# Performance work log

Measured on AMD Instinct MI355X. Metric: run time of the kernel, lower is better.

Reference implementation:

```python
import jax, jax.numpy as jnp
import numpy as np
import math

DIM = 1024
N_HEAD = 16
HEAD_DIM = DIM // N_HEAD  # 64
B, T = 4, 2048


def rotate_half(x):
    # lucidrains-style interleaved rotation: (x1, x2) pairs -> (-x2, x1)
    x = x.reshape(*x.shape[:-1], -1, 2)
    x1, x2 = x[..., 0], x[..., 1]
    return jnp.stack((-x2, x1), axis=-1).reshape(*x.shape[:-2], -1)


def apply_rope(x):
    # x: [b, h, t, d]
    d = x.shape[-1]
    t = x.shape[-2]
    inv_freq = 1.0 / (10000.0 ** (jnp.arange(0, d, 2, dtype=jnp.float32) / d))  # [d/2]
    angles = jnp.arange(t, dtype=jnp.float32)[:, None] * inv_freq[None, :]      # [t, d/2]
    angles = jnp.repeat(angles, 2, axis=-1)                                     # [t, d] interleaved
    cos, sin = jnp.cos(angles), jnp.sin(angles)
    return x * cos + rotate_half(x) * sin


def setup_inputs() -> dict:
    key = jax.random.key(0)
    kx, kw1, kb1, kw2, kb2 = jax.random.split(key, 5)
    x = jax.random.normal(kx, (B, T, DIM), dtype=jnp.float32)
    mask = jnp.tril(jnp.ones((T, T), dtype=jnp.int32))  # causal
    s = 0.02
    qkv_w = jax.random.normal(kw1, (DIM, 3 * DIM), dtype=jnp.float32) * s
    qkv_b = jax.random.normal(kb1, (3 * DIM,), dtype=jnp.float32) * s
    out_w = jax.random.normal(kw2, (DIM, DIM), dtype=jnp.float32) * s
    out_b = jax.random.normal(kb2, (DIM,), dtype=jnp.float32) * s
    return {"x": x, "mask": mask, "qkv_w": qkv_w, "qkv_b": qkv_b,
            "out_w": out_w, "out_b": out_b}


def reference(x, mask, qkv_w, qkv_b, out_w, out_b):
    b, t, _ = x.shape
    qkv = x @ qkv_w + qkv_b                       # [b, t, 3*dim]
    q, k, v = jnp.split(qkv, 3, axis=-1)
    def to_heads(z):
        return z.reshape(b, t, N_HEAD, HEAD_DIM).transpose(0, 2, 1, 3)  # [b,h,t,d]
    q, k, v = to_heads(q), to_heads(k), to_heads(v)
    q = apply_rope(q)
    k = apply_rope(k)
    scores = jnp.einsum('bhqd,bhkd->bhqk', q, k) / math.sqrt(HEAD_DIM)
    scores = jnp.where(mask[None, None, :, :] == 0, -jnp.inf, scores)
    attn = jax.nn.softmax(scores, axis=-1)        # dropout = identity (eval)
    out = jnp.einsum('bhqk,bhkd->bhqd', attn, v)  # [b,h,t,d]
    out = out.transpose(0, 2, 1, 3).reshape(b, t, DIM)
    return out @ out_w + out_b
```

## Files before the change

kernel.cpp:

```cpp
#include <hip/hip_runtime.h>

typedef __bf16 bf16_t;
typedef __bf16 bf16x8 __attribute__((ext_vector_type(8)));
typedef float  f32x4  __attribute__((ext_vector_type(4)));
typedef float  f32x16 __attribute__((ext_vector_type(16)));
typedef unsigned u32x4 __attribute__((ext_vector_type(4)));

#define DIMM  1024
#define NHEAD 16
#define HDIM  64
#define BATCH 4
#define SEQ   2048
#define MROWS (BATCH*SEQ)

#define AQB   128
#define AKV   64
#define NP    (SEQ/AQB)
#define SKS   72
#define LOG2E 1.44269504088896f

__device__ const int d_qb[24] = {15,15,7,14,14,13,13,6,12,12,11,11,5,10,10,9,9,4,8,8,3,2,1,0};
__device__ const int d_hh[24] = { 0, 1,2, 0, 1, 0, 1,2, 0, 1, 0, 1,2, 0, 1,0,1,2,0,1,2,2,2,2};

__device__ __forceinline__ void gload_lds16(const bf16_t* g, bf16_t* l) {
  __builtin_amdgcn_global_load_lds(
      (const __attribute__((address_space(1))) void*)g,
      (__attribute__((address_space(3))) void*)l, 16, 0, 0);
}

__device__ __forceinline__ unsigned short f2bu(float f) {
  bf16_t b = (bf16_t)f;
  return __builtin_bit_cast(unsigned short, b);
}
__device__ __forceinline__ float bu2f(unsigned short u) {
  return __uint_as_float(((unsigned)u) << 16);
}
__device__ __forceinline__ unsigned packbf(float a, float b) {
  return (unsigned)f2bu(a) | ((unsigned)f2bu(b) << 16);
}
__device__ __forceinline__ float fexp2(float x) {
  float r; asm("v_exp_f32 %0, %1" : "=v"(r) : "v"(x)); return r;
}

__global__ void k_convert(const float* __restrict__ in, bf16_t* __restrict__ out, int n4,
                          float* __restrict__ cosT, float* __restrict__ sinT) {
  int i = blockIdx.x * blockDim.x + threadIdx.x;
  if (i < n4) {
    float4 v = reinterpret_cast<const float4*>(in)[i];
    ushort4 o;
    o.x = f2bu(v.x); o.y = f2bu(v.y); o.z = f2bu(v.z); o.w = f2bu(v.w);
    reinterpret_cast<ushort4*>(out)[i] = o;
  } else {
    int id = i - n4;
    if (id < SEQ * 32) {
      int t = id >> 5, j = id & 31;
      double ang = (double)t * pow(10000.0, -(double)j / 32.0);
      cosT[id] = (float)cos(ang);
      sinT[id] = (float)sin(ang);
    }
  }
}

__global__ void k_transpose_convert(const float* __restrict__ in, bf16_t* __restrict__ out,
                                    int R, int C) {
  __shared__ float tile[32][33];
  int cb = blockIdx.x * 32, rb = blockIdx.y * 32;
  int tx = threadIdx.x, ty = threadIdx.y;
  #pragma unroll
  for (int i = 0; i < 4; ++i)
    tile[ty + i*8][tx] = in[(size_t)(rb + ty + i*8) * C + cb + tx];
  __syncthreads();
  #pragma unroll
  for (int i = 0; i < 4; ++i)
    out[(size_t)(cb + ty + i*8) * R + rb + tx] = (bf16_t)tile[tx][ty + i*8];
}

__global__ __launch_bounds__(512, 2) void k_gemm0(
    const bf16_t* __restrict__ A, const bf16_t* __restrict__ BT,
    const float* __restrict__ bias,
    bf16_t* __restrict__ q, bf16_t* __restrict__ k, bf16_t* __restrict__ vt,
    const float* __restrict__ cosT, const float* __restrict__ sinT)
{
  __shared__ bf16_t sA[2][2][128 * 64];
  __shared__ bf16_t sB[2][2][128 * 64];

  const int tid = threadIdx.x;
  const int w = tid >> 6;
  const int lane = tid & 63;
  const int wm = w >> 2, wn = w & 3;
  const int l15 = lane & 15, l4 = lane >> 4;

  int nwg = gridDim.x * gridDim.y;
  int id  = blockIdx.y * gridDim.x + blockIdx.x;
  int cpx = nwg >> 3;
  int sid = (id & 7) * cpx + (id >> 3);
  int bx = sid % gridDim.x, by = sid / gridDim.x;
  const int rowA0 = by * 256, colB0 = bx * 256;

  f32x4 acc[8][4] = {};
  bf16x8 bf_[4];

  auto stage = [&](int tile, int part) {
    if (tile >= 16) return;
    const int kh = part >> 1;
    const bool isB = part & 1;
    const bf16_t* src = isB ? BT : A;
    const int r0 = isB ? colB0 : rowA0;
    bf16_t* dst = (isB ? &sB[0][0][0] : &sA[0][0][0]) + ((tile & 1) * 2 + kh) * (128 * 64);
    #pragma unroll
    for (int call = 0; call < 2; ++call) {
      int n = call * 512 + tid;
      int R = n >> 3, slot = n & 7;
      int sp = slot ^ (R & 7);
      int row = R * 2 + (sp >> 2);
      gload_lds16(src + (size_t)(r0 + row) * 1024 + tile * 64 + kh * 32 + (sp & 3) * 8,
                  dst + n * 8);
    }
  };

  auto rdA = [&](int bc, int kh, int mfa) -> bf16x8 {
    int row = wm * 128 + mfa * 16 + l15;
    int R = row >> 1;
    int slot = (((row & 1) << 2) | l4) ^ (R & 7);
    return *reinterpret_cast<const bf16x8*>(&sA[bc][kh][R * 64 + slot * 8]);
  };
  auto rdB = [&](int bc, int kh, int nf) -> bf16x8 {
    int row = wn * 64 + nf * 16 + l15;
    int R = row >> 1;
    int slot = (((row & 1) << 2) | l4) ^ (R & 7);
    return *reinterpret_cast<const bf16x8*>(&sB[bc][kh][R * 64 + slot * 8]);
  };

  auto phase = [&](int bc, int kh, int mh, int stile, int spart, int wait_n) {
    bf16x8 af[4];
    if (mh == 0) {
      #pragma unroll
      for (int nf = 0; nf < 4; ++nf) bf_[nf] = rdB(bc, kh, nf);
    }
    #pragma unroll
    for (int mf = 0; mf < 4; ++mf) af[mf] = rdA(bc, kh, mh * 4 + mf);
    stage(stile, spart);
    if (wait_n == 4)      asm volatile("s_waitcnt vmcnt(4)" ::: "memory");
    else if (wait_n == 0) asm volatile("s_waitcnt vmcnt(0)" ::: "memory");
    __builtin_amdgcn_s_barrier();
    __builtin_amdgcn_s_setprio(1);
    #pragma unroll
    for (int mf = 0; mf < 4; ++mf)
      #pragma unroll
      for (int nf = 0; nf < 4; ++nf)
        acc[mh * 4 + mf][nf] = __builtin_amdgcn_mfma_f32_16x16x32_bf16(
            af[mf], bf_[nf], acc[mh * 4 + mf][nf], 0, 0, 0);
    __builtin_amdgcn_s_setprio(0);
    __builtin_amdgcn_s_barrier();
  };

  stage(0, 0); stage(0, 1); stage(0, 2); stage(0, 3);
  stage(1, 0); stage(1, 1);
  asm volatile("s_waitcnt vmcnt(4)" ::: "memory");
  __builtin_amdgcn_s_barrier();

  for (int i = 0; i < 8; ++i) {
    const int t0 = 2 * i, t1 = 2 * i + 1;
    phase(0, 0, 0, t1,     2, -1);
    phase(0, 0, 1, t1,     3, -1);
    phase(0, 1, 0, t0 + 2, 0, -1);
    phase(0, 1, 1, t0 + 2, 1, (t0 + 2 < 16) ? 4 : 0);
    phase(1, 0, 0, t0 + 2, 2, -1);
    phase(1, 0, 1, t0 + 2, 3, -1);
    phase(1, 1, 0, t0 + 3, 0, -1);
    phase(1, 1, 1, t0 + 3, 1, (t0 + 3 < 16) ? 4 : 0);
  }

  const bool isV = (bx >= 8);
  const bool isQ = (bx < 4);
  const float qs = 0.125f * LOG2E;
  if (isV) {
    #pragma unroll
    for (int mfa = 0; mfa < 8; ++mfa) {
      #pragma unroll
      for (int nf = 0; nf < 4; ++nf) {
        int n = colB0 + wn * 64 + nf * 16 + l15;
        int h = (n >> 6) & 15, d = n & 63;
        float bs = bias[n];
        int m0 = rowA0 + wm * 128 + mfa * 16 + l4 * 4;
        int b = m0 >> 11, t = m0 & 2047;
        ushort4 pk;
        pk.x = f2bu(acc[mfa][nf][0] + bs);
        pk.y = f2bu(acc[mfa][nf][1] + bs);
        pk.z = f2bu(acc[mfa][nf][2] + bs);
        pk.w = f2bu(acc[mfa][nf][3] + bs);
        *reinterpret_cast<ushort4*>(
            vt + ((size_t)((b * NHEAD + h) * HDIM + d)) * SEQ + t) = pk;
      }
    }
  } else {
    bf16_t* dst = isQ ? q : k;
    #pragma unroll
    for (int mfa = 0; mfa < 8; ++mfa) {
      #pragma unroll
      for (int nf = 0; nf < 4; ++nf) {
        int n = colB0 + wn * 64 + nf * 16 + l15;
        int h = (n >> 6) & 15, d = n & 63;
        int i2 = d >> 1;
        float bs = bias[n];
        #pragma unroll
        for (int r = 0; r < 4; ++r) {
          int m = rowA0 + wm * 128 + mfa * 16 + l4 * 4 + r;
          int b = m >> 11, t = m & 2047;
          float val = acc[mfa][nf][r] + bs;
          float prt = __shfl_xor(val, 1);
          float c = cosT[(t << 5) + i2], s = sinT[(t << 5) + i2];
          float y = (d & 1) ? (val * c + prt * s) : (val * c - prt * s);
          if (isQ) y *= qs;
          dst[((size_t)(b * NHEAD + h) * SEQ + t) * HDIM + d] = (bf16_t)y;
        }
      }
    }
  }
}

__global__ __launch_bounds__(256) void k_gemm1(
    const bf16_t* __restrict__ A, const bf16_t* __restrict__ BT,
    const float* __restrict__ bias, float* __restrict__ outf, int M, int N, int K)
{
  __shared__ bf16_t sA[128 * 32];
  __shared__ bf16_t sB[128 * 32];
  const int tid = threadIdx.x;
  const int w = tid >> 6, lane = tid & 63;
  const int wr = w >> 1, wc = w & 1;
  const int l15 = lane & 15, l4 = lane >> 4;

  int nwg = gridDim.x * gridDim.y;
  int id  = blockIdx.y * gridDim.x + blockIdx.x;
  int cpx = nwg >> 3;
  int sid = (id & 7) * cpx + (id >> 3);
  int bx = sid % gridDim.x, by = sid / gridDim.x;

  const int rowA0 = by * 128;
  const int colB0 = bx * 128;

  f32x4 acc[4][4] = {};

  const int nkt = K >> 5;
  for (int kt = 0; kt < nkt; ++kt) {
    __syncthreads();
    #pragma unroll
    for (int i = 0; i < 2; ++i) {
      int c = i * 256 + w * 64 + lane;
      int row = c >> 2, k8 = (c & 3) * 8;
      gload_lds16(A  + (size_t)(rowA0 + row) * K + kt * 32 + k8, sA + (i * 256 + w * 64) * 8);
      gload_lds16(BT + (size_t)(colB0 + row) * K + kt * 32 + k8, sB + (i * 256 + w * 64) * 8);
    }
    asm volatile("s_waitcnt vmcnt(0)" ::: "memory");
    __syncthreads();
    bf16x8 af[4], bfr[4];
    #pragma unroll
    for (int mi = 0; mi < 4; ++mi)
      af[mi] = *reinterpret_cast<const bf16x8*>(sA + (wr * 64 + mi * 16 + l15) * 32 + l4 * 8);
    #pragma unroll
    for (int ni = 0; ni < 4; ++ni)
      bfr[ni] = *reinterpret_cast<const bf16x8*>(sB + (wc * 64 + ni * 16 + l15) * 32 + l4 * 8);
    #pragma unroll
    for (int mi = 0; mi < 4; ++mi)
      #pragma unroll
      for (int ni = 0; ni < 4; ++ni)
        acc[mi][ni] = __builtin_amdgcn_mfma_f32_16x16x32_bf16(af[mi], bfr[ni], acc[mi][ni], 0, 0, 0);
  }

  #pragma unroll
  for (int mi = 0; mi < 4; ++mi) {
    #pragma unroll
    for (int ni = 0; ni < 4; ++ni) {
      int n = colB0 + wc * 64 + ni * 16 + l15;
      float bs = bias[n];
      #pragma unroll
      for (int r = 0; r < 4; ++r) {
        int m = rowA0 + wr * 64 + mi * 16 + l4 * 4 + r;
        outf[(size_t)m * N + n] = acc[mi][ni][r] + bs;
      }
    }
  }
}

#define ATTN_BODY(CBUF, T)                                                     \
  do {                                                                         \
    const int t_ = (T);                                                        \
    if (t_ + 1 < t1) {                                                         \
      asm volatile("s_waitcnt vmcnt(0)" ::: "memory");                         \
      stage(CBUF ^ 1);                                                         \
      if (t_ + 2 < t1) issue(t_ + 2);                                          \
    }                                                                          \
    const bool masked = (t_ * AKV + AKV - 1 > qbase);                          \
    f32x16 s0 = {}, s1 = {};                                                   \
    __builtin_amdgcn_s_setprio(1);                                             \
    _Pragma("unroll")                                                          \
    for (int kt = 0; kt < 4; ++kt) {                                           \
      bf16x8 kf0 = *reinterpret_cast<const bf16x8*>(                           \
          &sK[CBUF][l31 * SKS + (((2 * kt + hi) ^ (l31 >> 3)) << 3)]);         \
      s0 = __builtin_amdgcn_mfma_f32_32x32x16_bf16(kf0, qf[kt], s0, 0, 0, 0);  \
    }                                                                          \
    _Pragma("unroll")                                                          \
    for (int kt = 0; kt < 4; ++kt) {                                           \
      int kr1 = 32 + l31;                                                      \
      bf16x8 kf1 = *reinterpret_cast<const bf16x8*>(                           \
          &sK[CBUF][kr1 * SKS + (((2 * kt + hi) ^ (kr1 >> 3)) << 3)]);         \
      s1 = __builtin_amdgcn_mfma_f32_32x32x16_bf16(kf1, qf[kt], s1, 0, 0, 0);  \
    }                                                                          \
    __builtin_amdgcn_s_setprio(0);                                             \
    const int qa = qbase + l31;                                                \
    const int kb0 = t_ * AKV + 4 * hi;                                         \
    if (masked) {                                                              \
      _Pragma("unroll")                                                        \
      for (int r = 0; r < 16; ++r) {                                           \
        int kvi = kb0 + (r & 3) + 8 * (r >> 2);                                \
        if (kvi > qa) s0[r] = -1e30f;                                          \
        if (kvi + 32 > qa) s1[r] = -1e30f;                                     \
      }                                                                        \
    }                                                                          \
    float mm[16];                                                              \
    _Pragma("unroll")                                                          \
    for (int r = 0; r < 16; ++r) mm[r] = fmaxf(s0[r], s1[r]);                  \
    float m0_ = fmaxf(fmaxf(mm[0],  mm[1]),  mm[2]);                           \
    float m1_ = fmaxf(fmaxf(mm[3],  mm[4]),  mm[5]);                           \
    float m2_ = fmaxf(fmaxf(mm[6],  mm[7]),  mm[8]);                           \
    float m3_ = fmaxf(fmaxf(mm[9],  mm[10]), mm[11]);                          \
    float m4_ = fmaxf(fmaxf(mm[12], mm[13]), mm[14]);                          \
    float mt = fmaxf(fmaxf(fmaxf(m0_, m1_), fmaxf(m2_, m3_)), fmaxf(m4_, mm[15])); \
    mt = fmaxf(mt, __shfl_xor(mt, 32));                                        \
    if (!__all(mt <= mrun + 11.54f)) {                                         \
      float mnew = fmaxf(mrun, mt);                                            \
      float scl = fexp2(mrun - mnew);                                          \
      mrun = mnew;                                                             \
      lrun *= scl;                                                             \
      _Pragma("unroll")                                                        \
      for (int i = 0; i < 16; ++i) { accO[0][i] *= scl; accO[1][i] *= scl; }   \
    }                                                                          \
    float rs = 0.f;                                                            \
    _Pragma("unroll")                                                          \
    for (int r = 0; r < 16; ++r) { s0[r] = fexp2(s0[r] - mrun); rs += s0[r]; } \
    _Pragma("unroll")                                                          \
    for (int r = 0; r < 16; ++r) { s1[r] = fexp2(s1[r] - mrun); rs += s1[r]; } \
    lrun += rs;            \
    bf16x8 pf[4];                                                              \
    _Pragma("unroll")                                                          \
    for (int ktt = 0; ktt < 4; ++ktt) {                                        \
      const int bb = 8 * (ktt & 1);                                            \
      unsigned P01, P23, P45, P67;                                             \
      if (ktt < 2) {                                                           \
        P01 = packbf(s0[bb+0], s0[bb+1]); P23 = packbf(s0[bb+2], s0[bb+3]);    \
        P45 = packbf(s0[bb+4], s0[bb+5]); P67 = packbf(s0[bb+6], s0[bb+7]);    \
      } else {                                                                 \
        P01 = packbf(s1[bb+0], s1[bb+1]); P23 = packbf(s1[bb+2], s1[bb+3]);    \
        P45 = packbf(s1[bb+4], s1[bb+5]); P67 = packbf(s1[bb+6], s1[bb+7]);    \
      }                                                                        \
      unsigned ra = __shfl_xor(hi == 0 ? P45 : P01, 32);                       \
      unsigned rb = __shfl_xor(hi == 0 ? P67 : P23, 32);                       \
      unsigned dw0 = hi == 0 ? P01 : ra;                                       \
      unsigned dw1 = hi == 0 ? P23 : rb;                                       \
      unsigned dw2 = hi == 0 ? ra : P45;                                       \
      unsigned dw3 = hi == 0 ? rb : P67;                                       \
      pf[ktt] = __builtin_bit_cast(bf16x8, (u32x4){dw0, dw1, dw2, dw3});       \
    }                                                                          \
    __builtin_amdgcn_s_setprio(1);                                             \
    _Pragma("unroll")                                                          \
    for (int dt = 0; dt < 2; ++dt) {                                           \
      _Pragma("unroll")                                                        \
      for (int ktt = 0; ktt < 4; ++ktt) {                                      \
        int vrow = 32 * dt + l31;                                              \
        int slot = (4 * (ktt >> 1) + 2 * (ktt & 1) + hi) ^ (vrow >> 3);        \
        bf16x8 vf = *reinterpret_cast<const bf16x8*>(                          \
            &sV[CBUF][vrow * SKS + (slot << 3)]);                              \
        accO[dt] = __builtin_amdgcn_mfma_f32_32x32x16_bf16(vf, pf[ktt], accO[dt], 0, 0, 0); \
      }                                                                        \
    }                                                                          \
    __builtin_amdgcn_s_setprio(0);                                             \
    asm volatile("s_waitcnt lgkmcnt(0)" ::: "memory");                         \
    __builtin_amdgcn_s_barrier();                                              \
    asm volatile("" ::: "memory");                                             \
  } while (0)

__global__ __launch_bounds__(256, 2) void k_attn(
    const bf16_t* __restrict__ Q, const bf16_t* __restrict__ Kb,
    const bf16_t* __restrict__ Vt, bf16_t* __restrict__ O,
    bf16_t* __restrict__ Opart, float* __restrict__ ml)
{
  __shared__ bf16_t sK[2][64 * SKS];
  __shared__ bf16_t sV[2][64 * SKS];

  const int tid = threadIdx.x;
  const int w = tid >> 6, lane = tid & 63;
  const int l31 = lane & 31, hi = lane >> 5;

  const int id = blockIdx.x;
  const int cls = id >> 6;
  const int bh = id & 63;
  const int qblk = d_qb[cls];
  const int hh = d_hh[cls];
  const int ntf = 2 * qblk + 2;
  const int t0 = (hh == 1) ? (ntf >> 1) : 0;
  const int t1 = (hh == 0) ? (ntf >> 1) : ntf;

  const size_t hbase = (size_t)bh * SEQ * HDIM;
  const int b = bh >> 4, h = bh & 15;
  const int srow = tid >> 3, sslot = tid & 7;

  const int qbase = qblk * AQB + 32 * w;

  bf16x8 qf[4];
  #pragma unroll
  for (int kt = 0; kt < 4; ++kt)
    qf[kt] = *reinterpret_cast<const bf16x8*>(
        Q + hbase + (size_t)(qbase + l31) * HDIM + kt * 16 + hi * 8);
  asm volatile("s_waitcnt vmcnt(0)" ::: "memory");
  asm volatile("" : "+v"(qf[0]), "+v"(qf[1]), "+v"(qf[2]), "+v"(qf[3]));

  u32x4 kr[2], vr[2];
  auto issue = [&](int t) {
    const bf16_t* kp = Kb + hbase + (size_t)(t * AKV + srow) * HDIM + sslot * 8;
    const bf16_t* vp = Vt + hbase + (size_t)srow * SEQ + t * AKV + sslot * 8;
    asm volatile("global_load_dwordx4 %0, %1, off" : "=v"(kr[0]) : "v"(kp));
    asm volatile("global_load_dwordx4 %0, %1, off" : "=v"(kr[1]) : "v"(kp + 32 * HDIM));
    asm volatile("global_load_dwordx4 %0, %1, off" : "=v"(vr[0]) : "v"(vp));
    asm volatile("global_load_dwordx4 %0, %1, off" : "=v"(vr[1]) : "v"(vp + 32 * SEQ));
  };
  auto stage = [&](int nb) {
    #pragma unroll
    for (int cc = 0; cc < 2; ++cc) {
      int row = srow + 32 * cc;
      *reinterpret_cast<u32x4*>(&sK[nb][row * SKS + ((sslot ^ (row >> 3)) << 3)]) = kr[cc];
      *reinterpret_cast<u32x4*>(&sV[nb][row * SKS + ((sslot ^ (row >> 3)) << 3)]) = vr[cc];
    }
  };

  float mrun = -1e30f, lrun = 0.f;
  f32x16 accO[2] = {};

  issue(t0);
  asm volatile("s_waitcnt vmcnt(0)" ::: "memory");
  stage(0);
  if (t0 + 1 < t1) issue(t0 + 1);
  asm volatile("s_waitcnt lgkmcnt(0)" ::: "memory");
  __builtin_amdgcn_s_barrier();
  asm volatile("" ::: "memory");

  int t = t0;
  if ((t1 - t0) & 1) {
    ATTN_BODY(0, t); ++t;
    for (; t < t1; t += 2) { ATTN_BODY(1, t); ATTN_BODY(0, t + 1); }
  } else {
    for (; t < t1; t += 2) { ATTN_BODY(0, t); ATTN_BODY(1, t + 1); }
  }

  lrun += __shfl_xor(lrun, 32);

  bf16_t* sOw = &sK[0][0] + w * (32 * SKS);
  float inv = 1.f / lrun;
  #pragma unroll
  for (int dt = 0; dt < 2; ++dt)
    #pragma unroll
    for (int r = 0; r < 16; ++r) {
      int d = 32 * dt + (r & 3) + 8 * (r >> 2) + 4 * hi;
      sOw[l31 * SKS + (d ^ ((l31 >> 3) << 3))] = (bf16_t)(accO[dt][r] * inv);
    }
  if (hh == 2) {
    #pragma unroll
    for (int i = 0; i < 4; ++i) {
      int qr = 8 * i + (lane >> 3);
      int ch = lane & 7;
      bf16x8 vvv = *reinterpret_cast<const bf16x8*>(
          &sOw[qr * SKS + ((ch ^ (qr >> 3)) << 3)]);
      *reinterpret_cast<bf16x8*>(
          O + ((size_t)(b * SEQ + qbase + qr)) * DIMM + h * HDIM + ch * 8) = vvv;
    }
  } else {
    const int pb = ((qblk - 8) * 2 + hh) * 64 + bh;
    #pragma unroll
    for (int i = 0; i < 4; ++i) {
      int qr = 8 * i + (lane >> 3);
      int ch = lane & 7;
      bf16x8 vvv = *reinterpret_cast<const bf16x8*>(
          &sOw[qr * SKS + ((ch ^ (qr >> 3)) << 3)]);
      *reinterpret_cast<bf16x8*>(
          Opart + ((size_t)pb * 128 + 32 * w + qr) * 64 + ch * 8) = vvv;
    }
    if (hi == 0) {
      size_t mi = ((size_t)pb * 128 + 32 * w + l31) * 2;
      ml[mi] = mrun; ml[mi + 1] = lrun;
    }
  }
}

__global__ __launch_bounds__(256) void k_merge(
    const bf16_t* __restrict__ Opart, const float* __restrict__ ml,
    bf16_t* __restrict__ O)
{
  int blk = blockIdx.x;
  int qi = blk >> 6;
  int bh = blk & 63;
  int b = bh >> 4, h = bh & 15;
  int qblk = qi + 8;
  int base0 = (qi * 2 + 0) * 64 + bh;
  int base1 = (qi * 2 + 1) * 64 + bh;
  int q = threadIdx.x >> 1;
  int d0 = (threadIdx.x & 1) * 32;

  float m0 = ml[((size_t)base0 * 128 + q) * 2], l0 = ml[((size_t)base0 * 128 + q) * 2 + 1];
  float m1 = ml[((size_t)base1 * 128 + q) * 2], l1 = ml[((size_t)base1 * 128 + q) * 2 + 1];
  float m = fmaxf(m0, m1);
  float w0 = fexp2(m0 - m) * l0;
  float w1 = fexp2(m1 - m) * l1;
  float inv = 1.f / (w0 + w1);
  w0 *= inv; w1 *= inv;

  const bf16_t* p0 = Opart + ((size_t)base0 * 128 + q) * 64 + d0;
  const bf16_t* p1 = Opart + ((size_t)base1 * 128 + q) * 64 + d0;
  bf16_t* po = O + ((size_t)(b * SEQ + qblk * 128 + q)) * DIMM + h * HDIM + d0;
  #pragma unroll
  for (int i = 0; i < 4; ++i) {
    bf16x8 a = *reinterpret_cast<const bf16x8*>(p0 + i * 8);
    bf16x8 c = *reinterpret_cast<const bf16x8*>(p1 + i * 8);
    bf16x8 o;
    #pragma unroll
    for (int j = 0; j < 8; ++j)
      o[j] = (bf16_t)(w0 * (float)a[j] + w1 * (float)c[j]);
    *reinterpret_cast<bf16x8*>(po + i * 8) = o;
  }
}

extern "C" void kernel_launch(void* const* d_in, const int* in_sizes, int n_in,
                              void* d_out, int out_size, void* d_ws, size_t ws_size,
                              hipStream_t stream) {
  const float* x     = (const float*)d_in[0];
  const float* qkv_w = (const float*)d_in[2];
  const float* qkv_b = (const float*)d_in[3];
  const float* out_w = (const float*)d_in[4];
  const float* out_b = (const float*)d_in[5];
  float* out = (float*)d_out;

  char* ws = (char*)d_ws;
  size_t off = 0;
  auto alloc = [&](size_t bytes) {
    char* p = ws + off;
    off += (bytes + 255) & ~(size_t)255;
    return (void*)p;
  };
  bf16_t* Xb    = (bf16_t*)alloc((size_t)MROWS * DIMM * 2);
  bf16_t* WqkvT = (bf16_t*)alloc((size_t)3 * DIMM * DIMM * 2);
  bf16_t* WoutT = (bf16_t*)alloc((size_t)DIMM * DIMM * 2);
  bf16_t* Qh    = (bf16_t*)alloc((size_t)64 * SEQ * HDIM * 2);
  bf16_t* Kh    = (bf16_t*)alloc((size_t)64 * SEQ * HDIM * 2);
  bf16_t* Vth   = (bf16_t*)alloc((size_t)64 * HDIM * SEQ * 2);
  bf16_t* AO    = (bf16_t*)alloc((size_t)MROWS * DIMM * 2);
  float*  cosT  = (float*)alloc((size_t)SEQ * 32 * 4);
  float*  sinT  = (float*)alloc((size_t)SEQ * 32 * 4);
  float*  mlbuf = (float*)alloc((size_t)16 * 64 * 128 * 2 * 4);
  bf16_t* Opart = Xb;

  const int n4 = MROWS * DIMM / 4;
  k_convert<<<(n4 + SEQ * 32 + 255) / 256, 256, 0, stream>>>(x, Xb, n4, cosT, sinT);
  k_transpose_convert<<<dim3(3 * DIMM / 32, DIMM / 32), dim3(32, 8), 0, stream>>>(qkv_w, WqkvT, DIMM, 3 * DIMM);
  k_transpose_convert<<<dim3(DIMM / 32, DIMM / 32), dim3(32, 8), 0, stream>>>(out_w, WoutT, DIMM, DIMM);

  k_gemm0<<<dim3(3 * DIMM / 256, MROWS / 256), 512, 0, stream>>>(
      Xb, WqkvT, qkv_b, Qh, Kh, Vth, cosT, sinT);

  k_attn<<<dim3(24 * 64), 256, 0, stream>>>(Qh, Kh, Vth, AO, Opart, mlbuf);

  k_merge<<<dim3(512), 256, 0, stream>>>(Opart, mlbuf, AO);

  k_gemm1<<<dim3(DIMM / 128, MROWS / 128), 256, 0, stream>>>(
      AO, WoutT, out_b, out, MROWS, DIMM, DIMM);
}
```

Measured before the change: 193.4 us.

## Interleave two paired attention work items per block to overlap softmax and MFMA

Each attention block now processes two complementary (q-block, split) work classes at once, chosen from a pairing table so the two items' combined KV tile counts are roughly balanced. Each item gets its own double-buffered K/V LDS tiles, Q fragments, running max/sum and accumulators. Per iteration the QK MFMAs of both streams are issued before their softmax and PV phases, so one stream's exp/max work can overlap the other's matrix ops. The grid is halved, and one barrier is shared per iteration. In exchange, LDS use per block doubles and register pressure rises sharply under launch_bounds(256,2), which risks spills or lower occupancy.

```diff
diff --git a/kernel.cpp b/kernel.cpp
--- a/kernel.cpp
+++ b/kernel.cpp
@@ -21,6 +21,7 @@
 
 __device__ const int d_qb[24] = {15,15,7,14,14,13,13,6,12,12,11,11,5,10,10,9,9,4,8,8,3,2,1,0};
 __device__ const int d_hh[24] = { 0, 1,2, 0, 1, 0, 1,2, 0, 1, 0, 1,2, 0, 1,0,1,2,0,1,2,2,2,2};
+__device__ const int d_pa[12] = {4,6,7,9,11,3,5,8,10,2,1,0};
 
 __device__ __forceinline__ void gload_lds16(const bf16_t* g, bf16_t* l) {
   __builtin_amdgcn_global_load_lds(
@@ -282,101 +283,155 @@
   }
 }
 
-#define ATTN_BODY(CBUF, T)                                                     \
+#define ISSUE_J(krj, vrj, tj)                                                  \
   do {                                                                         \
-    const int t_ = (T);                                                        \
-    if (t_ + 1 < t1) {                                                         \
-      asm volatile("s_waitcnt vmcnt(0)" ::: "memory");                         \
-      stage(CBUF ^ 1);                                                         \
-      if (t_ + 2 < t1) issue(t_ + 2);                                          \
-    }                                                                          \
-    const bool masked = (t_ * AKV + AKV - 1 > qbase);                          \
-    f32x16 s0 = {}, s1 = {};                                                   \
+    const bf16_t* kp_ = Kb + hbase + (size_t)((tj) * AKV + srow) * HDIM + sslot * 8; \
+    const bf16_t* vp_ = Vt + hbase + (size_t)srow * SEQ + (tj) * AKV + sslot * 8; \
+    asm volatile("global_load_dwordx4 %0, %1, off" : "=v"(krj[0]) : "v"(kp_)); \
+    asm volatile("global_load_dwordx4 %0, %1, off" : "=v"(krj[1]) : "v"(kp_ + 32 * HDIM)); \
+    asm volatile("global_load_dwordx4 %0, %1, off" : "=v"(vrj[0]) : "v"(vp_)); \
+    asm volatile("global_load_dwordx4 %0, %1, off" : "=v"(vrj[1]) : "v"(vp_ + 32 * SEQ)); \
+  } while (0)
+
+#define STAGE_J(sKj, sVj, nb, krj, vrj)                                        \
+  do {                                                                         \
+    _Pragma("unroll")                                                          \
+    for (int cc_ = 0; cc_ < 2; ++cc_) {                                        \
+      int row_ = srow + 32 * cc_;                                              \
+      *reinterpret_cast<u32x4*>(&sKj[nb][row_ * SKS + ((sslot ^ (row_ >> 3)) << 3)]) = krj[cc_]; \
+      *reinterpret_cast<u32x4*>(&sVj[nb][row_ * SKS + ((sslot ^ (row_ >> 3)) << 3)]) = vrj[cc_]; \
+    }                                                                          \
+  } while (0)
+
+#define QK_J(sKj, cb, qfj, s0j, s1j)                                           \
+  do {                                                                         \
     __builtin_amdgcn_s_setprio(1);                                             \
     _Pragma("unroll")                                                          \
-    for (int kt = 0; kt < 4; ++kt) {                                           \
-      bf16x8 kf0 = *reinterpret_cast<const bf16x8*>(                           \
-          &sK[CBUF][l31 * SKS + (((2 * kt + hi) ^ (l31 >> 3)) << 3)]);         \
-      s0 = __builtin_amdgcn_mfma_f32_32x32x16_bf16(kf0, qf[kt], s0, 0, 0, 0);  \
-    }                                                                          \
-    _Pragma("unroll")                                                          \
-    for (int kt = 0; kt < 4; ++kt) {                                           \
-      int kr1 = 32 + l31;                                                      \
-      bf16x8 kf1 = *reinterpret_cast<const bf16x8*>(                           \
-          &sK[CBUF][kr1 * SKS + (((2 * kt + hi) ^ (kr1 >> 3)) << 3)]);         \
-      s1 = __builtin_amdgcn_mfma_f32_32x32x16_bf16(kf1, qf[kt], s1, 0, 0, 0);  \
+    for (int kt_ = 0; kt_ < 4; ++kt_) {                                        \
+      bf16x8 kf_ = *reinterpret_cast<const bf16x8*>(                           \
+          &sKj[cb][l31 * SKS + (((2 * kt_ + hi) ^ (l31 >> 3)) << 3)]);         \
+      s0j = __builtin_amdgcn_mfma_f32_32x32x16_bf16(kf_, qfj[kt_], s0j, 0, 0, 0); \
+    }                                                                          \
+    _Pragma("unroll")                                                          \
+    for (int kt_ = 0; kt_ < 4; ++kt_) {                                        \
+      int kr_ = 32 + l31;                                                      \
+      bf16x8 kf_ = *reinterpret_cast<const bf16x8*>(                           \
+          &sKj[cb][kr_ * SKS + (((2 * kt_ + hi) ^ (kr_ >> 3)) << 3)]);         \
+      s1j = __builtin_amdgcn_mfma_f32_32x32x16_bf16(kf_, qfj[kt_], s1j, 0, 0, 0); \
     }                                                                          \
     __builtin_amdgcn_s_setprio(0);                                             \
-    const int qa = qbase + l31;                                                \
-    const int kb0 = t_ * AKV + 4 * hi;                                         \
-    if (masked) {                                                              \
+  } while (0)
+
+#define SMPV_J(sVj, cb, tj, qbasej, s0j, s1j, mrunj, lrunj, accj)              \
+  do {                                                                         \
+    const bool masked_ = ((tj) * AKV + AKV - 1 > (qbasej));                    \
+    const int qa_ = (qbasej) + l31;                                            \
+    const int kb0_ = (tj) * AKV + 4 * hi;                                      \
+    if (masked_) {                                                             \
       _Pragma("unroll")                                                        \
-      for (int r = 0; r < 16; ++r) {                                           \
-        int kvi = kb0 + (r & 3) + 8 * (r >> 2);                                \
-        if (kvi > qa) s0[r] = -1e30f;                                          \
-        if (kvi + 32 > qa) s1[r] = -1e30f;                                     \
-      }                                                                        \
-    }                                                                          \
-    float mm[16];                                                              \
-    _Pragma("unroll")                                                          \
-    for (int r = 0; r < 16; ++r) mm[r] = fmaxf(s0[r], s1[r]);                  \
-    float m0_ = fmaxf(fmaxf(mm[0],  mm[1]),  mm[2]);                           \
-    float m1_ = fmaxf(fmaxf(mm[3],  mm[4]),  mm[5]);                           \
-    float m2_ = fmaxf(fmaxf(mm[6],  mm[7]),  mm[8]);                           \
-    float m3_ = fmaxf(fmaxf(mm[9],  mm[10]), mm[11]);                          \
-    float m4_ = fmaxf(fmaxf(mm[12], mm[13]), mm[14]);                          \
-    float mt = fmaxf(fmaxf(fmaxf(m0_, m1_), fmaxf(m2_, m3_)), fmaxf(m4_, mm[15])); \
-    mt = fmaxf(mt, __shfl_xor(mt, 32));                                        \
-    if (!__all(mt <= mrun + 11.54f)) {                                         \
-      float mnew = fmaxf(mrun, mt);                                            \
-      float scl = fexp2(mrun - mnew);                                          \
-      mrun = mnew;                                                             \
-      lrun *= scl;                                                             \
+      for (int r_ = 0; r_ < 16; ++r_) {                                        \
+        int kvi_ = kb0_ + (r_ & 3) + 8 * (r_ >> 2);                            \
+        if (kvi_ > qa_) s0j[r_] = -1e30f;                                      \
+        if (kvi_ + 32 > qa_) s1j[r_] = -1e30f;                                 \
+      }                                                                        \
+    }                                                                          \
+    float mm_[16];                                                             \
+    _Pragma("unroll")                                                          \
+    for (int r_ = 0; r_ < 16; ++r_) mm_[r_] = fmaxf(s0j[r_], s1j[r_]);         \
+    float a0_ = fmaxf(fmaxf(mm_[0],  mm_[1]),  mm_[2]);                        \
+    float a1_ = fmaxf(fmaxf(mm_[3],  mm_[4]),  mm_[5]);                        \
+    float a2_ = fmaxf(fmaxf(mm_[6],  mm_[7]),  mm_[8]);                        \
+    float a3_ = fmaxf(fmaxf(mm_[9],  mm_[10]), mm_[11]);                       \
+    float a4_ = fmaxf(fmaxf(mm_[12], mm_[13]), mm_[14]);                       \
+    float mt_ = fmaxf(fmaxf(fmaxf(a0_, a1_), fmaxf(a2_, a3_)), fmaxf(a4_, mm_[15])); \
+    mt_ = fmaxf(mt_, __shfl_xor(mt_, 32));                                     \
+    if (!__all(mt_ <= mrunj + 11.54f)) {                                       \
+      float mn_ = fmaxf(mrunj, mt_);                                           \
+      float sc_ = fexp2(mrunj - mn_);                                          \
+      mrunj = mn_;                                                             \
+      lrunj *= sc_;                                                            \
       _Pragma("unroll")                                                        \
-      for (int i = 0; i < 16; ++i) { accO[0][i] *= scl; accO[1][i] *= scl; }   \
-    }                                                                          \
-    float rs = 0.f;                                                            \
-    _Pragma("unroll")                                                          \
-    for (int r = 0; r < 16; ++r) { s0[r] = fexp2(s0[r] - mrun); rs += s0[r]; } \
-    _Pragma("unroll")                                                          \
-    for (int r = 0; r < 16; ++r) { s1[r] = fexp2(s1[r] - mrun); rs += s1[r]; } \
-    lrun += rs;            \
-    bf16x8 pf[4];                                                              \
-    _Pragma("unroll")                                                          \
-    for (int ktt = 0; ktt < 4; ++ktt) {                                        \
-      const int bb = 8 * (ktt & 1);                                            \
-      unsigned P01, P23, P45, P67;                                             \
-      if (ktt < 2) {                                                           \
-        P01 = packbf(s0[bb+0], s0[bb+1]); P23 = packbf(s0[bb+2], s0[bb+3]);    \
-        P45 = packbf(s0[bb+4], s0[bb+5]); P67 = packbf(s0[bb+6], s0[bb+7]);    \
+      for (int i_ = 0; i_ < 16; ++i_) { accj[0][i_] *= sc_; accj[1][i_] *= sc_; } \
+    }                                                                          \
+    float rs_ = 0.f;                                                           \
+    _Pragma("unroll")                                                          \
+    for (int r_ = 0; r_ < 16; ++r_) { s0j[r_] = fexp2(s0j[r_] - mrunj); rs_ += s0j[r_]; } \
+    _Pragma("unroll")                                                          \
+    for (int r_ = 0; r_ < 16; ++r_) { s1j[r_] = fexp2(s1j[r_] - mrunj); rs_ += s1j[r_]; } \
+    lrunj += rs_;                                                              \
+    bf16x8 pf_[4];                                                             \
+    _Pragma("unroll")                                                          \
+    for (int kt_ = 0; kt_ < 4; ++kt_) {                                        \
+      const int bb_ = 8 * (kt_ & 1);                                           \
+      unsigned P01_, P23_, P45_, P67_;                                         \
+      if (kt_ < 2) {                                                           \
+        P01_ = packbf(s0j[bb_+0], s0j[bb_+1]); P23_ = packbf(s0j[bb_+2], s0j[bb_+3]); \
+        P45_ = packbf(s0j[bb_+4], s0j[bb_+5]); P67_ = packbf(s0j[bb_+6], s0j[bb_+7]); \
       } else {                                                                 \
-        P01 = packbf(s1[bb+0], s1[bb+1]); P23 = packbf(s1[bb+2], s1[bb+3]);    \
-        P45 = packbf(s1[bb+4], s1[bb+5]); P67 = packbf(s1[bb+6], s1[bb+7]);    \
-      }                                                                        \
-      unsigned ra = __shfl_xor(hi == 0 ? P45 : P01, 32);                       \
-      unsigned rb = __shfl_xor(hi == 0 ? P67 : P23, 32);                       \
-      unsigned dw0 = hi == 0 ? P01 : ra;                                       \
-      unsigned dw1 = hi == 0 ? P23 : rb;                                       \
-      unsigned dw2 = hi == 0 ? ra : P45;                                       \
-      unsigned dw3 = hi == 0 ? rb : P67;                                       \
-      pf[ktt] = __builtin_bit_cast(bf16x8, (u32x4){dw0, dw1, dw2, dw3});       \
+        P01_ = packbf(s1j[bb_+0], s1j[bb_+1]); P23_ = packbf(s1j[bb_+2], s1j[bb_+3]); \
+        P45_ = packbf(s1j[bb_+4], s1j[bb_+5]); P67_ = packbf(s1j[bb_+6], s1j[bb_+7]); \
+      }                                                                        \
+      unsigned ra_ = __shfl_xor(hi == 0 ? P45_ : P01_, 32);                    \
+      unsigned rb_ = __shfl_xor(hi == 0 ? P67_ : P23_, 32);                    \
+      unsigned d0_ = hi == 0 ? P01_ : ra_;                                     \
+      unsigned d1_ = hi == 0 ? P23_ : rb_;                                     \
+      unsigned d2_ = hi == 0 ? ra_ : P45_;                                     \
+      unsigned d3_ = hi == 0 ? rb_ : P67_;                                     \
+      pf_[kt_] = __builtin_bit_cast(bf16x8, (u32x4){d0_, d1_, d2_, d3_});      \
     }                                                                          \
     __builtin_amdgcn_s_setprio(1);                                             \
     _Pragma("unroll")                                                          \
-    for (int dt = 0; dt < 2; ++dt) {                                           \
+    for (int dt_ = 0; dt_ < 2; ++dt_) {                                        \
       _Pragma("unroll")                                                        \
-      for (int ktt = 0; ktt < 4; ++ktt) {                                      \
-        int vrow = 32 * dt + l31;                                              \
-        int slot = (4 * (ktt >> 1) + 2 * (ktt & 1) + hi) ^ (vrow >> 3);        \
-        bf16x8 vf = *reinterpret_cast<const bf16x8*>(                          \
-            &sV[CBUF][vrow * SKS + (slot << 3)]);                              \
-        accO[dt] = __builtin_amdgcn_mfma_f32_32x32x16_bf16(vf, pf[ktt], accO[dt], 0, 0, 0); \
+      for (int kt_ = 0; kt_ < 4; ++kt_) {                                      \
+        int vr_ = 32 * dt_ + l31;                                              \
+        int sl_ = (4 * (kt_ >> 1) + 2 * (kt_ & 1) + hi) ^ (vr_ >> 3);          \
+        bf16x8 vf_ = *reinterpret_cast<const bf16x8*>(                         \
+            &sVj[cb][vr_ * SKS + (sl_ << 3)]);                                 \
+        accj[dt_] = __builtin_amdgcn_mfma_f32_32x32x16_bf16(vf_, pf_[kt_], accj[dt_], 0, 0, 0); \
       }                                                                        \
     }                                                                          \
     __builtin_amdgcn_s_setprio(0);                                             \
+  } while (0)
+
+#define EPI_J(hhj, qbj, qbasej, mrunj, lrunj, accj)                            \
+  do {                                                                         \
+    lrunj += __shfl_xor(lrunj, 32);                                            \
+    float inv_ = 1.f / lrunj;                                                  \
+    _Pragma("unroll")                                                          \
+    for (int dt_ = 0; dt_ < 2; ++dt_)                                          \
+      _Pragma("unroll")                                                        \
+      for (int r_ = 0; r_ < 16; ++r_) {                                        \
+        int d_ = 32 * dt_ + (r_ & 3) + 8 * (r_ >> 2) + 4 * hi;                 \
+        sOw[l31 * SKS + (d_ ^ ((l31 >> 3) << 3))] = (bf16_t)(accj[dt_][r_] * inv_); \
+      }                                                                        \
+    if ((hhj) == 2) {                                                          \
+      _Pragma("unroll")                                                        \
+      for (int i_ = 0; i_ < 4; ++i_) {                                         \
+        int qr_ = 8 * i_ + (lane >> 3);                                        \
+        int ch_ = lane & 7;                                                    \
+        bf16x8 vv_ = *reinterpret_cast<const bf16x8*>(                         \
+            &sOw[qr_ * SKS + ((ch_ ^ (qr_ >> 3)) << 3)]);                      \
+        *reinterpret_cast<bf16x8*>(                                            \
+            O + ((size_t)(b * SEQ + (qbasej) + qr_)) * DIMM + h * HDIM + ch_ * 8) = vv_; \
+      }                                                                        \
+    } else {                                                                   \
+      const int pb_ = (((qbj) - 8) * 2 + (hhj)) * 64 + bh;                     \
+      _Pragma("unroll")                                                        \
+      for (int i_ = 0; i_ < 4; ++i_) {                                         \
+        int qr_ = 8 * i_ + (lane >> 3);                                        \
+        int ch_ = lane & 7;                                                    \
+        bf16x8 vv_ = *reinterpret_cast<const bf16x8*>(                         \
+            &sOw[qr_ * SKS + ((ch_ ^ (qr_ >> 3)) << 3)]);                      \
+        *reinterpret_cast<bf16x8*>(                                            \
+            Opart + ((size_t)pb_ * 128 + 32 * w + qr_) * 64 + ch_ * 8) = vv_;  \
+      }                                                                        \
+      if (hi == 0) {                                                           \
+        size_t mi_ = ((size_t)pb_ * 128 + 32 * w + l31) * 2;                   \
+        ml[mi_] = mrunj; ml[mi_ + 1] = lrunj;                                  \
+      }                                                                        \
+    }                                                                          \
     asm volatile("s_waitcnt lgkmcnt(0)" ::: "memory");                         \
-    __builtin_amdgcn_s_barrier();                                              \
-    asm volatile("" ::: "memory");                                             \
   } while (0)
 
 __global__ __launch_bounds__(256, 2) void k_attn(
@@ -384,110 +439,79 @@
     const bf16_t* __restrict__ Vt, bf16_t* __restrict__ O,
     bf16_t* __restrict__ Opart, float* __restrict__ ml)
 {
-  __shared__ bf16_t sK[2][64 * SKS];
-  __shared__ bf16_t sV[2][64 * SKS];
+  __shared__ bf16_t sKA[2][64 * SKS], sVA[2][64 * SKS];
+  __shared__ bf16_t sKB[2][64 * SKS], sVB[2][64 * SKS];
 
   const int tid = threadIdx.x;
   const int w = tid >> 6, lane = tid & 63;
   const int l31 = lane & 31, hi = lane >> 5;
-
-  const int id = blockIdx.x;
-  const int cls = id >> 6;
-  const int bh = id & 63;
-  const int qblk = d_qb[cls];
-  const int hh = d_hh[cls];
-  const int ntf = 2 * qblk + 2;
-  const int t0 = (hh == 1) ? (ntf >> 1) : 0;
-  const int t1 = (hh == 0) ? (ntf >> 1) : ntf;
+  const int srow = tid >> 3, sslot = tid & 7;
+
+  const int pr = blockIdx.x >> 6, bh = blockIdx.x & 63;
+  const int clsA = d_pa[pr], clsB = 23 - clsA;
+  const int qbA = d_qb[clsA], hhA = d_hh[clsA];
+  const int qbB = d_qb[clsB], hhB = d_hh[clsB];
+  const int ntA = 2 * qbA + 2, ntB = 2 * qbB + 2;
+  const int t0A = (hhA == 1) ? (ntA >> 1) : 0;
+  const int t1A = (hhA == 0) ? (ntA >> 1) : ntA;
+  const int t0B = (hhB == 1) ? (ntB >> 1) : 0;
+  const int t1B = (hhB == 0) ? (ntB >> 1) : ntB;
+  const int nA = t1A - t0A, nB = t1B - t0B;
+  const int nmax = nA > nB ? nA : nB;
 
   const size_t hbase = (size_t)bh * SEQ * HDIM;
   const int b = bh >> 4, h = bh & 15;
-  const int srow = tid >> 3, sslot = tid & 7;
-
-  const int qbase = qblk * AQB + 32 * w;
-
-  bf16x8 qf[4];
+  const int qbaseA = qbA * AQB + 32 * w;
+  const int qbaseB = qbB * AQB + 32 * w;
+
+  bf16x8 qfA[4], qfB[4];
   #pragma unroll
-  for (int kt = 0; kt < 4; ++kt)
-    qf[kt] = *reinterpret_cast<const bf16x8*>(
-        Q + hbase + (size_t)(qbase + l31) * HDIM + kt * 16 + hi * 8);
+  for (int kt = 0; kt < 4; ++kt) {
+    qfA[kt] = *reinterpret_cast<const bf16x8*>(
+        Q + hbase + (size_t)(qbaseA + l31) * HDIM + kt * 16 + hi * 8);
+    qfB[kt] = *reinterpret_cast<const bf16x8*>(
+        Q + hbase + (size_t)(qbaseB + l31) * HDIM + kt * 16 + hi * 8);
+  }
   asm volatile("s_waitcnt vmcnt(0)" ::: "memory");
-  asm volatile("" : "+v"(qf[0]), "+v"(qf[1]), "+v"(qf[2]), "+v"(qf[3]));
-
-  u32x4 kr[2], vr[2];
-  auto issue = [&](int t) {
-    const bf16_t* kp = Kb + hbase + (size_t)(t * AKV + srow) * HDIM + sslot * 8;
-    const bf16_t* vp = Vt + hbase + (size_t)srow * SEQ + t * AKV + sslot * 8;
-    asm volatile("global_load_dwordx4 %0, %1, off" : "=v"(kr[0]) : "v"(kp));
-    asm volatile("global_load_dwordx4 %0, %1, off" : "=v"(kr[1]) : "v"(kp + 32 * HDIM));
-    asm volatile("global_load_dwordx4 %0, %1, off" : "=v"(vr[0]) : "v"(vp));
-    asm volatile("global_load_dwordx4 %0, %1, off" : "=v"(vr[1]) : "v"(vp + 32 * SEQ));
-  };
-  auto stage = [&](int nb) {
-    #pragma unroll
-    for (int cc = 0; cc < 2; ++cc) {
-      int row = srow + 32 * cc;
-      *reinterpret_cast<u32x4*>(&sK[nb][row * SKS + ((sslot ^ (row >> 3)) << 3)]) = kr[cc];
-      *reinterpret_cast<u32x4*>(&sV[nb][row * SKS + ((sslot ^ (row >> 3)) << 3)]) = vr[cc];
-    }
-  };
-
-  float mrun = -1e30f, lrun = 0.f;
-  f32x16 accO[2] = {};
-
-  issue(t0);
+
+  u32x4 krA[2], vrA[2], krB[2], vrB[2];
+  float mrunA = -1e30f, lrunA = 0.f, mrunB = -1e30f, lrunB = 0.f;
+  f32x16 accA[2] = {}, accB[2] = {};
+
+  ISSUE_J(krA, vrA, t0A);
+  ISSUE_J(krB, vrB, t0B);
   asm volatile("s_waitcnt vmcnt(0)" ::: "memory");
-  stage(0);
-  if (t0 + 1 < t1) issue(t0 + 1);
+  STAGE_J(sKA, sVA, 0, krA, vrA);
+  STAGE_J(sKB, sVB, 0, krB, vrB);
+  if (nA > 1) ISSUE_J(krA, vrA, t0A + 1);
+  if (nB > 1) ISSUE_J(krB, vrB, t0B + 1);
   asm volatile("s_waitcnt lgkmcnt(0)" ::: "memory");
   __builtin_amdgcn_s_barrier();
   asm volatile("" ::: "memory");
 
-  int t = t0;
-  if ((t1 - t0) & 1) {
-    ATTN_BODY(0, t); ++t;
-    for (; t < t1; t += 2) { ATTN_BODY(1, t); ATTN_BODY(0, t + 1); }
-  } else {
-    for (; t < t1; t += 2) { ATTN_BODY(0, t); ATTN_BODY(1, t + 1); }
-  }
-
-  lrun += __shfl_xor(lrun, 32);
-
-  bf16_t* sOw = &sK[0][0] + w * (32 * SKS);
-  float inv = 1.f / lrun;
-  #pragma unroll
-  for (int dt = 0; dt < 2; ++dt)
-    #pragma unroll
-    for (int r = 0; r < 16; ++r) {
-      int d = 32 * dt + (r & 3) + 8 * (r >> 2) + 4 * hi;
-      sOw[l31 * SKS + (d ^ ((l31 >> 3) << 3))] = (bf16_t)(accO[dt][r] * inv);
-    }
-  if (hh == 2) {
-    #pragma unroll
-    for (int i = 0; i < 4; ++i) {
-      int qr = 8 * i + (lane >> 3);
-      int ch = lane & 7;
-      bf16x8 vvv = *reinterpret_cast<const bf16x8*>(
-          &sOw[qr * SKS + ((ch ^ (qr >> 3)) << 3)]);
-      *reinterpret_cast<bf16x8*>(
-          O + ((size_t)(b * SEQ + qbase + qr)) * DIMM + h * HDIM + ch * 8) = vvv;
-    }
-  } else {
-    const int pb = ((qblk - 8) * 2 + hh) * 64 + bh;
-    #pragma unroll
-    for (int i = 0; i < 4; ++i) {
-      int qr = 8 * i + (lane >> 3);
-      int ch = lane & 7;
-      bf16x8 vvv = *reinterpret_cast<const bf16x8*>(
-          &sOw[qr * SKS + ((ch ^ (qr >> 3)) << 3)]);
-      *reinterpret_cast<bf16x8*>(
-          Opart + ((size_t)pb * 128 + 32 * w + qr) * 64 + ch * 8) = vvv;
-    }
-    if (hi == 0) {
-      size_t mi = ((size_t)pb * 128 + 32 * w + l31) * 2;
-      ml[mi] = mrun; ml[mi + 1] = lrun;
-    }
-  }
+  for (int i = 0; i < nmax; ++i) {
+    const int c = i & 1;
+    const bool aAct = i < nA, bAct = i < nB;
+    asm volatile("s_waitcnt vmcnt(0)" ::: "memory");
+    if (aAct && i + 1 < nA) STAGE_J(sKA, sVA, c ^ 1, krA, vrA);
+    if (bAct && i + 1 < nB) STAGE_J(sKB, sVB, c ^ 1, krB, vrB);
+    if (aAct && i + 2 < nA) ISSUE_J(krA, vrA, t0A + i + 2);
+    if (bAct && i + 2 < nB) ISSUE_J(krB, vrB, t0B + i + 2);
+
+    f32x16 s0A = {}, s1A = {}, s0B = {}, s1B = {};
+    if (aAct) QK_J(sKA, c, qfA, s0A, s1A);
+    if (bAct) QK_J(sKB, c, qfB, s0B, s1B);
+    if (aAct) SMPV_J(sVA, c, t0A + i, qbaseA, s0A, s1A, mrunA, lrunA, accA);
+    if (bAct) SMPV_J(sVB, c, t0B + i, qbaseB, s0B, s1B, mrunB, lrunB, accB);
+
+    asm volatile("s_waitcnt lgkmcnt(0)" ::: "memory");
+    __builtin_amdgcn_s_barrier();
+    asm volatile("" ::: "memory");
+  }
+
+  bf16_t* sOw = &sKA[0][0] + w * (32 * SKS);
+  EPI_J(hhA, qbA, qbaseA, mrunA, lrunA, accA);
+  EPI_J(hhB, qbB, qbaseB, mrunB, lrunB, accB);
 }
 
 __global__ __launch_bounds__(256) void k_merge(
@@ -564,7 +588,7 @@
   k_gemm0<<<dim3(3 * DIMM / 256, MROWS / 256), 512, 0, stream>>>(
       Xb, WqkvT, qkv_b, Qh, Kh, Vth, cosT, sinT);
 
-  k_attn<<<dim3(24 * 64), 256, 0, stream>>>(Qh, Kh, Vth, AO, Opart, mlbuf);
+  k_attn<<<dim3(12 * 64), 256, 0, stream>>>(Qh, Kh, Vth, AO, Opart, mlbuf);
 
   k_merge<<<dim3(512), 256, 0, stream>>>(Opart, mlbuf, AO);
 
```

New measurement: 205.8 us. 6.4% more time.

## Retile QKV GEMM to 256x192 tiles with restructured double-buffered pipeline

Applied to the files above, without the earlier changes.

Changes the QKV projection GEMM tile from 256x256 to 256x192, giving 512 workgroups (16x32) instead of 384. That spreads the work across the compute units more evenly. The K-loop is rewritten as a per-tile two-buffer pipeline with separate A and B staging and fewer barriers. The epilogue now picks the Q/K/V path per column, since a tile can span Q/K/V boundaries. Occupancy is lowered to 1 block per SM, and the smaller N tile reduces arithmetic intensity per tile.

```diff
diff --git a/kernel.cpp b/kernel.cpp
--- a/kernel.cpp
+++ b/kernel.cpp
@@ -75,14 +75,14 @@
     out[(size_t)(cb + ty + i*8) * R + rb + tx] = (bf16_t)tile[tx][ty + i*8];
 }
 
-__global__ __launch_bounds__(512, 2) void k_gemm0(
+__global__ __launch_bounds__(512, 1) void k_gemm0(
     const bf16_t* __restrict__ A, const bf16_t* __restrict__ BT,
     const float* __restrict__ bias,
     bf16_t* __restrict__ q, bf16_t* __restrict__ k, bf16_t* __restrict__ vt,
     const float* __restrict__ cosT, const float* __restrict__ sinT)
 {
   __shared__ bf16_t sA[2][2][128 * 64];
-  __shared__ bf16_t sB[2][2][128 * 64];
+  __shared__ bf16_t sB[2][2][96 * 64];
 
   const int tid = threadIdx.x;
   const int w = tid >> 6;
@@ -90,31 +90,38 @@
   const int wm = w >> 2, wn = w & 3;
   const int l15 = lane & 15, l4 = lane >> 4;
 
-  int nwg = gridDim.x * gridDim.y;
   int id  = blockIdx.y * gridDim.x + blockIdx.x;
-  int cpx = nwg >> 3;
-  int sid = (id & 7) * cpx + (id >> 3);
-  int bx = sid % gridDim.x, by = sid / gridDim.x;
-  const int rowA0 = by * 256, colB0 = bx * 256;
-
-  f32x4 acc[8][4] = {};
-  bf16x8 bf_[4];
-
-  auto stage = [&](int tile, int part) {
+  int sid = (id & 7) * 64 + (id >> 3);
+  int bx = sid % 16, by = sid / 16;
+  const int rowA0 = by * 256, colB0 = bx * 192;
+
+  f32x4 acc[8][3] = {};
+
+  auto stageA = [&](int tile, int kh) {
     if (tile >= 16) return;
-    const int kh = part >> 1;
-    const bool isB = part & 1;
-    const bf16_t* src = isB ? BT : A;
-    const int r0 = isB ? colB0 : rowA0;
-    bf16_t* dst = (isB ? &sB[0][0][0] : &sA[0][0][0]) + ((tile & 1) * 2 + kh) * (128 * 64);
+    bf16_t* dst = &sA[tile & 1][kh][0];
     #pragma unroll
     for (int call = 0; call < 2; ++call) {
       int n = call * 512 + tid;
       int R = n >> 3, slot = n & 7;
       int sp = slot ^ (R & 7);
       int row = R * 2 + (sp >> 2);
-      gload_lds16(src + (size_t)(r0 + row) * 1024 + tile * 64 + kh * 32 + (sp & 3) * 8,
+      gload_lds16(A + (size_t)(rowA0 + row) * 1024 + tile * 64 + kh * 32 + (sp & 3) * 8,
                   dst + n * 8);
+    }
+  };
+  auto stageB = [&](int tile) {
+    if (tile >= 16) return;
+    #pragma unroll
+    for (int call = 0; call < 3; ++call) {
+      int n = call * 512 + tid;
+      int kh = (n >= 768) ? 1 : 0;
+      int m = n - kh * 768;
+      int R = m >> 3, slot = m & 7;
+      int sp = slot ^ (R & 7);
+      int row = R * 2 + (sp >> 2);
+      gload_lds16(BT + (size_t)(colB0 + row) * 1024 + tile * 64 + kh * 32 + (sp & 3) * 8,
+                  &sB[tile & 1][kh][0] + m * 8);
     }
   };
 
@@ -125,63 +132,82 @@
     return *reinterpret_cast<const bf16x8*>(&sA[bc][kh][R * 64 + slot * 8]);
   };
   auto rdB = [&](int bc, int kh, int nf) -> bf16x8 {
-    int row = wn * 64 + nf * 16 + l15;
+    int row = wn * 48 + nf * 16 + l15;
     int R = row >> 1;
     int slot = (((row & 1) << 2) | l4) ^ (R & 7);
     return *reinterpret_cast<const bf16x8*>(&sB[bc][kh][R * 64 + slot * 8]);
   };
 
-  auto phase = [&](int bc, int kh, int mh, int stile, int spart, int wait_n) {
-    bf16x8 af[4];
-    if (mh == 0) {
-      #pragma unroll
-      for (int nf = 0; nf < 4; ++nf) bf_[nf] = rdB(bc, kh, nf);
-    }
-    #pragma unroll
-    for (int mf = 0; mf < 4; ++mf) af[mf] = rdA(bc, kh, mh * 4 + mf);
-    stage(stile, spart);
-    if (wait_n == 4)      asm volatile("s_waitcnt vmcnt(4)" ::: "memory");
-    else if (wait_n == 0) asm volatile("s_waitcnt vmcnt(0)" ::: "memory");
-    __builtin_amdgcn_s_barrier();
+  stageA(0, 0); stageA(0, 1); stageB(0); stageA(1, 0);
+  asm volatile("s_waitcnt vmcnt(2)" ::: "memory");
+  __builtin_amdgcn_s_barrier();
+
+  for (int t = 0; t < 16; ++t) {
+    const int bc = t & 1;
+    bf16x8 bfr[3], af[4];
+    #pragma unroll
+    for (int nf = 0; nf < 3; ++nf) bfr[nf] = rdB(bc, 0, nf);
+    #pragma unroll
+    for (int mf = 0; mf < 4; ++mf) af[mf] = rdA(bc, 0, mf);
+    stageA(t + 1, 1);
     __builtin_amdgcn_s_setprio(1);
     #pragma unroll
     for (int mf = 0; mf < 4; ++mf)
       #pragma unroll
-      for (int nf = 0; nf < 4; ++nf)
-        acc[mh * 4 + mf][nf] = __builtin_amdgcn_mfma_f32_16x16x32_bf16(
-            af[mf], bf_[nf], acc[mh * 4 + mf][nf], 0, 0, 0);
+      for (int nf = 0; nf < 3; ++nf)
+        acc[mf][nf] = __builtin_amdgcn_mfma_f32_16x16x32_bf16(
+            af[mf], bfr[nf], acc[mf][nf], 0, 0, 0);
+    __builtin_amdgcn_s_setprio(0);
+    #pragma unroll
+    for (int mf = 0; mf < 4; ++mf) af[mf] = rdA(bc, 0, 4 + mf);
+    stageB(t + 1);
+    __builtin_amdgcn_s_setprio(1);
+    #pragma unroll
+    for (int mf = 0; mf < 4; ++mf)
+      #pragma unroll
+      for (int nf = 0; nf < 3; ++nf)
+        acc[4 + mf][nf] = __builtin_amdgcn_mfma_f32_16x16x32_bf16(
+            af[mf], bfr[nf], acc[4 + mf][nf], 0, 0, 0);
     __builtin_amdgcn_s_setprio(0);
     __builtin_amdgcn_s_barrier();
-  };
-
-  stage(0, 0); stage(0, 1); stage(0, 2); stage(0, 3);
-  stage(1, 0); stage(1, 1);
-  asm volatile("s_waitcnt vmcnt(4)" ::: "memory");
-  __builtin_amdgcn_s_barrier();
-
-  for (int i = 0; i < 8; ++i) {
-    const int t0 = 2 * i, t1 = 2 * i + 1;
-    phase(0, 0, 0, t1,     2, -1);
-    phase(0, 0, 1, t1,     3, -1);
-    phase(0, 1, 0, t0 + 2, 0, -1);
-    phase(0, 1, 1, t0 + 2, 1, (t0 + 2 < 16) ? 4 : 0);
-    phase(1, 0, 0, t0 + 2, 2, -1);
-    phase(1, 0, 1, t0 + 2, 3, -1);
-    phase(1, 1, 0, t0 + 3, 0, -1);
-    phase(1, 1, 1, t0 + 3, 1, (t0 + 3 < 16) ? 4 : 0);
-  }
-
-  const bool isV = (bx >= 8);
-  const bool isQ = (bx < 4);
+    #pragma unroll
+    for (int nf = 0; nf < 3; ++nf) bfr[nf] = rdB(bc, 1, nf);
+    #pragma unroll
+    for (int mf = 0; mf < 4; ++mf) af[mf] = rdA(bc, 1, mf);
+    stageA(t + 2, 0);
+    __builtin_amdgcn_s_setprio(1);
+    #pragma unroll
+    for (int mf = 0; mf < 4; ++mf)
+      #pragma unroll
+      for (int nf = 0; nf < 3; ++nf)
+        acc[mf][nf] = __builtin_amdgcn_mfma_f32_16x16x32_bf16(
+            af[mf], bfr[nf], acc[mf][nf], 0, 0, 0);
+    __builtin_amdgcn_s_setprio(0);
+    #pragma unroll
+    for (int mf = 0; mf < 4; ++mf) af[mf] = rdA(bc, 1, 4 + mf);
+    __builtin_amdgcn_s_setprio(1);
+    #pragma unroll
+    for (int mf = 0; mf < 4; ++mf)
+      #pragma unroll
+      for (int nf = 0; nf < 3; ++nf)
+        acc[4 + mf][nf] = __builtin_amdgcn_mfma_f32_16x16x32_bf16(
+            af[mf], bfr[nf], acc[4 + mf][nf], 0, 0, 0);
+    __builtin_amdgcn_s_setprio(0);
+    if (t + 2 < 16) asm volatile("s_waitcnt vmcnt(2)" ::: "memory");
+    else            asm volatile("s_waitcnt vmcnt(0)" ::: "memory");
+    __builtin_amdgcn_s_barrier();
+  }
+
   const float qs = 0.125f * LOG2E;
-  if (isV) {
-    #pragma unroll
-    for (int mfa = 0; mfa < 8; ++mfa) {
-      #pragma unroll
-      for (int nf = 0; nf < 4; ++nf) {
-        int n = colB0 + wn * 64 + nf * 16 + l15;
-        int h = (n >> 6) & 15, d = n & 63;
-        float bs = bias[n];
+  #pragma unroll
+  for (int mfa = 0; mfa < 8; ++mfa) {
+    #pragma unroll
+    for (int nf = 0; nf < 3; ++nf) {
+      int n = colB0 + wn * 48 + nf * 16 + l15;
+      int which = n >> 10;
+      int h = (n >> 6) & 15, d = n & 63;
+      float bs = bias[n];
+      if (which == 2) {
         int m0 = rowA0 + wm * 128 + mfa * 16 + l4 * 4;
         int b = m0 >> 11, t = m0 & 2047;
         ushort4 pk;
@@ -191,18 +217,9 @@
         pk.w = f2bu(acc[mfa][nf][3] + bs);
         *reinterpret_cast<ushort4*>(
             vt + ((size_t)((b * NHEAD + h) * HDIM + d)) * SEQ + t) = pk;
-      }
-    }
-  } else {
-    bf16_t* dst = isQ ? q : k;
-    #pragma unroll
-    for (int mfa = 0; mfa < 8; ++mfa) {
-      #pragma unroll
-      for (int nf = 0; nf < 4; ++nf) {
-        int n = colB0 + wn * 64 + nf * 16 + l15;
-        int h = (n >> 6) & 15, d = n & 63;
+      } else {
+        bf16_t* dst = which ? k : q;
         int i2 = d >> 1;
-        float bs = bias[n];
         #pragma unroll
         for (int r = 0; r < 4; ++r) {
           int m = rowA0 + wm * 128 + mfa * 16 + l4 * 4 + r;
@@ -211,7 +228,7 @@
           float prt = __shfl_xor(val, 1);
           float c = cosT[(t << 5) + i2], s = sinT[(t << 5) + i2];
           float y = (d & 1) ? (val * c + prt * s) : (val * c - prt * s);
-          if (isQ) y *= qs;
+          if (which == 0) y *= qs;
           dst[((size_t)(b * NHEAD + h) * SEQ + t) * HDIM + d] = (bf16_t)y;
         }
       }
@@ -561,7 +578,7 @@
   k_transpose_convert<<<dim3(3 * DIMM / 32, DIMM / 32), dim3(32, 8), 0, stream>>>(qkv_w, WqkvT, DIMM, 3 * DIMM);
   k_transpose_convert<<<dim3(DIMM / 32, DIMM / 32), dim3(32, 8), 0, stream>>>(out_w, WoutT, DIMM, DIMM);
 
-  k_gemm0<<<dim3(3 * DIMM / 256, MROWS / 256), 512, 0, stream>>>(
+  k_gemm0<<<dim3(3 * DIMM / 192, MROWS / 256), 512, 0, stream>>>(
       Xb, WqkvT, qkv_b, Qh, Kh, Vth, cosT, sinT);
 
   k_attn<<<dim3(24 * 64), 256, 0, stream>>>(Qh, Kh, Vth, AO, Opart, mlbuf);
```

Result: no change. 194.4 us (+0.5%).
